# Optimization experiments

Hardware: AMD Instinct MI355X
Metric: run time of the kernel (lower is better)

Reference implementation:

```python
import jax, jax.numpy as jnp
import numpy as np

NUM_EMBEDDINGS = 512
PADDING_IDX = 0
MAX_POSITIONAL = 16
B, W, L = 128, 512, 16


def setup_inputs() -> dict:
    key = jax.random.key(0)
    k1, k2 = jax.random.split(key)
    token_ids = jax.random.randint(k1, (B, W, L), 0, NUM_EMBEDDINGS, dtype=jnp.int64 if jax.config.jax_enable_x64 else jnp.int32).astype(jnp.int32)
    position_ids = jax.random.randint(k2, (B, W, L), 0, MAX_POSITIONAL).astype(jnp.int32)
    return {"token_ids": token_ids, "position_ids": position_ids}


def reference(token_ids, position_ids):
    # token_ids, position_ids: (B, W, L) int
    b, w, l = token_ids.shape
    d = NUM_EMBEDDINGS + MAX_POSITIONAL
    tok = token_ids.reshape(b * w, l)
    pos = position_ids.reshape(b * w, l)
    m = (tok != PADDING_IDX).astype(jnp.float32)  # mask out padding chars
    rows = jnp.broadcast_to(jnp.arange(b * w)[:, None], (b * w, l))
    vecs = jnp.zeros((b * w, d), dtype=jnp.float32)
    # char-count histogram + positional-count histogram (offset by NUM_EMBEDDINGS)
    vecs = vecs.at[rows, tok].add(m)
    vecs = vecs.at[rows, NUM_EMBEDDINGS + pos].add(m)
    return vecs.reshape(b, w, d)
```

## Files before the change

kernel.cpp:

```cpp
#include <hip/hip_runtime.h>


constexpr int NUM_EMB = 512;
constexpr int MAX_POS = 16;
constexpr int D = NUM_EMB + MAX_POS;
constexpr int L = 16;
constexpr int ROWS_PER_BLOCK = 16;
constexpr int THREADS = 512;
constexpr int SCATTER = ROWS_PER_BLOCK * L;
constexpr int HIST = ROWS_PER_BLOCK * D;
constexpr int HIST4 = HIST / 4;
constexpr int FULL_IT = HIST4 / THREADS;
constexpr int REM = HIST4 - FULL_IT * THREADS;

typedef float v4f __attribute__((ext_vector_type(4)));

__global__ __launch_bounds__(THREADS)
void pcls_hist_kernel(const int* __restrict__ tok,
                      const int* __restrict__ pos,
                      float* __restrict__ out) {
    __shared__ float hist[HIST];

    const int tid = threadIdx.x;
    const long long row_base = (long long)blockIdx.x * ROWS_PER_BLOCK;

    int t = 0, p = 0;
    if (tid < SCATTER) {
        const long long g = row_base * L + tid;
        t = tok[g];
        p = pos[g];
    }

    v4f* h4 = reinterpret_cast<v4f*>(hist);
    #pragma unroll
    for (int i = 0; i < FULL_IT; ++i)
        h4[tid + i * THREADS] = (v4f)0.0f;
    if (tid < REM)
        h4[tid + FULL_IT * THREADS] = (v4f)0.0f;
    __syncthreads();

    if (tid < SCATTER && t != 0) {
        const int r = tid >> 4;
        atomicAdd(&hist[r * D + t], 1.0f);
        atomicAdd(&hist[r * D + NUM_EMB + p], 1.0f);
    }
    __syncthreads();

    v4f* out4 = reinterpret_cast<v4f*>(out + row_base * D);
    #pragma unroll
    for (int i = 0; i < FULL_IT; ++i)
        __builtin_nontemporal_store(h4[tid + i * THREADS], &out4[tid + i * THREADS]);
    if (tid < REM)
        __builtin_nontemporal_store(h4[tid + FULL_IT * THREADS],
                                    &out4[tid + FULL_IT * THREADS]);
}

extern "C" void kernel_launch(void* const* d_in, const int* in_sizes, int n_in,
                              void* d_out, int out_size, void* d_ws, size_t ws_size,
                              hipStream_t stream) {
    const int* tok = (const int*)d_in[0];
    const int* pos = (const int*)d_in[1];
    float* out = (float*)d_out;

    const int n_rows = in_sizes[0] / L;
    const int grid = n_rows / ROWS_PER_BLOCK;

    pcls_hist_kernel<<<grid, THREADS, 0, stream>>>(tok, pos, out);
}
```

Measured before the change: 151.4 us.

## Use grid-stride persistent blocks with prefetch of next row group's indices

The launch changes from one block per 16 rows to a fixed grid of 2048 blocks of 256 threads. Each block loops over four 8-row groups and prefetches the next group's token and position ids while the current histogram is built and stored. The aim is to cut block launch overhead and LDS footprint so more blocks stay resident, and to hide index load latency behind the output writes. In exchange, the row count is hard-coded instead of taken from the input sizes, and each block now does serialized work with an extra barrier per group.

```diff
diff --git a/kernel.cpp b/kernel.cpp
--- a/kernel.cpp
+++ b/kernel.cpp
@@ -5,13 +5,17 @@
 constexpr int MAX_POS = 16;
 constexpr int D = NUM_EMB + MAX_POS;
 constexpr int L = 16;
-constexpr int ROWS_PER_BLOCK = 16;
-constexpr int THREADS = 512;
-constexpr int SCATTER = ROWS_PER_BLOCK * L;
-constexpr int HIST = ROWS_PER_BLOCK * D;
+constexpr int RPG = 8;
+constexpr int THREADS = 256;
+constexpr int SCATTER = RPG * L;
+constexpr int HIST = RPG * D;
 constexpr int HIST4 = HIST / 4;
 constexpr int FULL_IT = HIST4 / THREADS;
 constexpr int REM = HIST4 - FULL_IT * THREADS;
+constexpr int NBLOCKS = 2048;
+constexpr int TOTAL_ROWS = 65536;
+constexpr int GROUPS = TOTAL_ROWS / RPG;
+constexpr int GPB = GROUPS / NBLOCKS;
 
 typedef float v4f __attribute__((ext_vector_type(4)));
 
@@ -22,37 +26,51 @@
     __shared__ float hist[HIST];
 
     const int tid = threadIdx.x;
-    const long long row_base = (long long)blockIdx.x * ROWS_PER_BLOCK;
+    int g = blockIdx.x;
 
     int t = 0, p = 0;
     if (tid < SCATTER) {
-        const long long g = row_base * L + tid;
-        t = tok[g];
-        p = pos[g];
+        const long long base = (long long)g * (RPG * L) + tid;
+        t = tok[base];
+        p = pos[base];
     }
 
     v4f* h4 = reinterpret_cast<v4f*>(hist);
+
     #pragma unroll
-    for (int i = 0; i < FULL_IT; ++i)
-        h4[tid + i * THREADS] = (v4f)0.0f;
-    if (tid < REM)
-        h4[tid + FULL_IT * THREADS] = (v4f)0.0f;
-    __syncthreads();
+    for (int it = 0; it < GPB; ++it) {
+        #pragma unroll
+        for (int i = 0; i < FULL_IT; ++i)
+            h4[tid + i * THREADS] = (v4f)0.0f;
+        if (tid < REM)
+            h4[tid + FULL_IT * THREADS] = (v4f)0.0f;
+        __syncthreads();
 
-    if (tid < SCATTER && t != 0) {
-        const int r = tid >> 4;
-        atomicAdd(&hist[r * D + t], 1.0f);
-        atomicAdd(&hist[r * D + NUM_EMB + p], 1.0f);
+        if (tid < SCATTER && t != 0) {
+            const int r = tid >> 4;
+            atomicAdd(&hist[r * D + t], 1.0f);
+            atomicAdd(&hist[r * D + NUM_EMB + p], 1.0f);
+        }
+
+        int tn = 0, pn = 0;
+        if (it + 1 < GPB && tid < SCATTER) {
+            const long long base = (long long)(g + NBLOCKS) * (RPG * L) + tid;
+            tn = tok[base];
+            pn = pos[base];
+        }
+        __syncthreads();
+
+        v4f* out4 = reinterpret_cast<v4f*>(out + (long long)g * (RPG * D));
+        #pragma unroll
+        for (int i = 0; i < FULL_IT; ++i)
+            __builtin_nontemporal_store(h4[tid + i * THREADS],
+                                        &out4[tid + i * THREADS]);
+        if (tid < REM)
+            __builtin_nontemporal_store(h4[tid + FULL_IT * THREADS],
+                                        &out4[tid + FULL_IT * THREADS]);
+
+        t = tn; p = pn; g += NBLOCKS;
     }
-    __syncthreads();
-
-    v4f* out4 = reinterpret_cast<v4f*>(out + row_base * D);
-    #pragma unroll
-    for (int i = 0; i < FULL_IT; ++i)
-        __builtin_nontemporal_store(h4[tid + i * THREADS], &out4[tid + i * THREADS]);
-    if (tid < REM)
-        __builtin_nontemporal_store(h4[tid + FULL_IT * THREADS],
-                                    &out4[tid + FULL_IT * THREADS]);
 }
 
 extern "C" void kernel_launch(void* const* d_in, const int* in_sizes, int n_in,
@@ -62,8 +80,5 @@
     const int* pos = (const int*)d_in[1];
     float* out = (float*)d_out;
 
-    const int n_rows = in_sizes[0] / L;
-    const int grid = n_rows / ROWS_PER_BLOCK;
-
-    pcls_hist_kernel<<<grid, THREADS, 0, stream>>>(tok, pos, out);
+    pcls_hist_kernel<<<NBLOCKS, THREADS, 0, stream>>>(tok, pos, out);
 }
```

New measurement: 153.6 us. About the same (+1.5%).
